# Optimization experiments

Measured on AMD Instinct MI355X. Metric: run time of the kernel, lower is better.

Reference implementation:

```python
import jax, jax.numpy as jnp
import numpy as np

N_NODES = 50000

def setup_inputs() -> dict:
    key = jax.random.key(0)
    k1, k2, k3, k4, k5 = jax.random.split(key, 5)
    x = jax.random.normal(k1, (50000, 512), dtype=jnp.float32)
    edge_row = jax.random.randint(k2, (800000,), 0, N_NODES, dtype=jnp.int64)
    edge_col = jax.random.randint(k3, (800000,), 0, N_NODES, dtype=jnp.int64)
    edge_val = jax.random.uniform(k4, (800000,), dtype=jnp.float32)
    # init like torch: uniform(-stdv, stdv), stdv = 1/sqrt(out_features)
    stdv = 1.0 / np.sqrt(96.0)
    weight = jax.random.uniform(k5, (512, 96), minval=-stdv, maxval=stdv, dtype=jnp.float32)
    return {"x": x, "edge_row": edge_row, "edge_col": edge_col, "edge_val": edge_val, "weight": weight}

def reference(x, edge_row, edge_col, edge_val, weight):
    # support = X @ W  -- dense GEMM [N, F_in] x [F_in, F_out]
    support = x @ weight
    # sparse adjacency matmul: out[row] += val * support[col]
    msgs = edge_val[:, None] * support[edge_col]          # [E, F_out]
    out = jax.ops.segment_sum(msgs, edge_row, num_segments=N_NODES)
    # act = ReLU (module default); bias=False
    return jax.nn.relu(out)
```

## Files before the change

kernel.cpp:

```cpp
#include <hip/hip_runtime.h>

#define N_NODES 50000
#define F_IN    512
#define F_OUT   96
#define N_EDGES 800000

#define RPB    128
#define NBKT   391
#define CAP    2560
#define ECHUNK 4096
#define NCHUNK ((N_EDGES + ECHUNK - 1) / ECHUNK)
#define GEMM_BLOCKS ((N_NODES + 63) / 64)

typedef __attribute__((ext_vector_type(8))) short bf16x8;
typedef __attribute__((ext_vector_type(4))) float f32x4;

__device__ __forceinline__ unsigned short f2bf(float f) {
    unsigned int u = __float_as_uint(f);
    unsigned int r = (u + 0x7FFFu + ((u >> 16) & 1u)) >> 16;
    return (unsigned short)r;
}
__device__ __forceinline__ float bf2f(unsigned short h) {
    return __uint_as_float(((unsigned int)h) << 16);
}

__global__ __launch_bounds__(256) void k_wcast(const float* __restrict__ w,
                                               unsigned short* __restrict__ wTq,
                                               int* __restrict__ bcnt) {
    if (blockIdx.x == 0) {
        const int t = threadIdx.x;
        bcnt[t] = 0;
        if (t < 144) bcnt[256 + t] = 0;
    }
    const int i = blockIdx.x * 256 + threadIdx.x;
    if (i < F_OUT * F_IN) {
        const int j    = i & 7;
        const int lane = (i >> 3) & 63;
        const int ks   = (i >> 9) & 1;
        const int tp   = i >> 10;
        const int t    = tp % 6;
        const int p    = tp / 6;
        const int lr   = lane & 15;
        const int kg   = lane >> 4;
        const int n    = t * 16 + lr;
        const int k    = p * 64 + ks * 32 + kg * 8 + j;
        wTq[i] = f2bf(w[(size_t)k * F_OUT + n]);
    }
}

__global__ __launch_bounds__(512) void k_fused(const float* __restrict__ x,
                                               const unsigned short* __restrict__ wTq,
                                               unsigned short* __restrict__ support,
                                               const int* __restrict__ erow,
                                               const int* __restrict__ ecol,
                                               const float* __restrict__ eval,
                                               int* __restrict__ bcnt,
                                               float2* __restrict__ bucket) {
    __shared__ __align__(16) char smem[16384];
    const int tid = threadIdx.x;

    if (blockIdx.x < NCHUNK) {
        int* hist  = (int*)smem;
        int* gbase = hist + 400;
        int* lcur  = gbase + 400;
        for (int i = tid; i < NBKT; i += 512) { hist[i] = 0; lcur[i] = 0; }
        __syncthreads();

        const int base = blockIdx.x * ECHUNK;
        const int n = min(ECHUNK, N_EDGES - base);

        for (int i = tid; i < n; i += 512)
            atomicAdd(&hist[erow[base + i] >> 7], 1);
        __syncthreads();

        for (int b = tid; b < NBKT; b += 512)
            gbase[b] = hist[b] ? atomicAdd(&bcnt[b], hist[b]) : 0;
        __syncthreads();

        for (int i = tid; i < n; i += 512) {
            const int r = erow[base + i];
            const int b = r >> 7;
            const int pos = gbase[b] + atomicAdd(&lcur[b], 1);
            if (pos >= 0 && pos < CAP)
                bucket[(size_t)b * CAP + pos] = make_float2(
                    __int_as_float(((r & 127) << 16) | ecol[base + i]),
                    eval[base + i]);
        }
        return;
    }

    unsigned short (*sX)[64 * 64] = (unsigned short (*)[64 * 64])smem;

    const int lane = tid & 63;
    const int wave = tid >> 6;
    const int wr   = wave & 3;
    const int wc   = wave >> 2;
    const int r0   = (blockIdx.x - NCHUNK) * 64;
    const int lr   = lane & 15;
    const int kg   = lane >> 4;

    f32x4 acc[3];
    #pragma unroll
    for (int t = 0; t < 3; ++t) acc[t] = (f32x4){0.f, 0.f, 0.f, 0.f};

    float4 xr[2];

    auto XLOAD = [&](int p) {
        #pragma unroll
        for (int i = 0; i < 2; ++i) {
            const int chunk = i * 512 + tid;
            const int row   = chunk >> 4;
            const int c     = chunk & 15;
            int gr = r0 + row;
            if (gr > N_NODES - 1) gr = N_NODES - 1;
            xr[i] = *reinterpret_cast<const float4*>(x + (size_t)gr * F_IN + p * 64 + c * 4);
        }
    };
    auto XWRITE = [&](int buf) {
        char* xb = (char*)&sX[buf][0];
        #pragma unroll
        for (int i = 0; i < 2; ++i) {
            const int chunk = i * 512 + tid;
            const int row   = chunk >> 4;
            const int c     = chunk & 15;
            ushort4 h;
            h.x = f2bf(xr[i].x); h.y = f2bf(xr[i].y);
            h.z = f2bf(xr[i].z); h.w = f2bf(xr[i].w);
            const int byte = (c * 8) ^ ((row & 7) << 4);
            *reinterpret_cast<ushort4*>(xb + row * 128 + byte) = h;
        }
    };
    auto COMPUTE = [&](int buf, int p) {
        const char* xb = (const char*)&sX[buf][0];
        const int xrow = wr * 16 + lr;
        const unsigned short* bbase = wTq + ((size_t)p * 12 + wc * 6) * 512 + lane * 8;
        #pragma unroll
        for (int ks = 0; ks < 2; ++ks) {
            const int off = (ks * 64 + kg * 16) ^ ((xrow & 7) << 4);
            const bf16x8 af = *reinterpret_cast<const bf16x8*>(xb + xrow * 128 + off);
            #pragma unroll
            for (int t = 0; t < 3; ++t) {
                const bf16x8 bq = *reinterpret_cast<const bf16x8*>(
                    bbase + (t * 2 + ks) * 512);
                acc[t] = __builtin_amdgcn_mfma_f32_16x16x32_bf16(af, bq, acc[t], 0, 0, 0);
            }
        }
    };

    XLOAD(0);
    XWRITE(0);
    __syncthreads();
    for (int p = 0; p < 8; ++p) {
        if (p < 7) XLOAD(p + 1);
        COMPUTE(p & 1, p);
        if (p < 7) XWRITE((p + 1) & 1);
        __syncthreads();
    }

    #pragma unroll
    for (int t = 0; t < 3; ++t) {
        #pragma unroll
        for (int r = 0; r < 4; ++r) {
            const int row = r0 + wr * 16 + kg * 4 + r;
            if (row < N_NODES)
                support[(size_t)row * F_OUT + wc * 48 + t * 16 + lr] = f2bf(acc[t][r]);
        }
    }
}

__global__ __launch_bounds__(256) void kS_sort(const int* __restrict__ bcnt,
                                               const float2* __restrict__ bucket,
                                               float2* __restrict__ bucket2,
                                               int* __restrict__ rowOffs) {
    __shared__ int cnt[RPB];
    __shared__ int sc[RPB];
    __shared__ int rbase[RPB];
    __shared__ int rcur[RPB];
    const int b   = blockIdx.x;
    const int tid = threadIdx.x;

    if (tid < RPB) { cnt[tid] = 0; rcur[tid] = 0; }
    __syncthreads();

    const int beg = b * CAP;
    const int n   = min(bcnt[b], CAP);

    for (int i = tid; i < n; i += 256)
        atomicAdd(&cnt[(__float_as_int(bucket[beg + i].x) >> 16) & 127], 1);
    __syncthreads();

    if (tid < RPB) sc[tid] = cnt[tid];
    __syncthreads();
    #pragma unroll
    for (int off = 1; off < RPB; off <<= 1) {
        int a = 0;
        if (tid < RPB && tid >= off) a = sc[tid - off];
        __syncthreads();
        if (tid < RPB) sc[tid] += a;
        __syncthreads();
    }
    if (tid < RPB) {
        const int rb = beg + sc[tid] - cnt[tid];
        rbase[tid] = rb;
        rowOffs[b * 129 + tid] = rb;
    }
    if (tid == RPB) rowOffs[b * 129 + RPB] = beg + n;
    __syncthreads();

    for (int i = tid; i < n; i += 256) {
        const float2 ev  = bucket[beg + i];
        const int    key = __float_as_int(ev.x);
        const int    r   = (key >> 16) & 127;
        const int    pos = rbase[r] + atomicAdd(&rcur[r], 1);
        bucket2[pos] = make_float2(__int_as_float(key & 0xFFFF), ev.y);
    }
}

__global__ __launch_bounds__(256) void k_gather(const int* __restrict__ rowOffs,
                                                const float2* __restrict__ bucket2,
                                                const unsigned short* __restrict__ support,
                                                float* __restrict__ out) {
    const int gid = blockIdx.x * 256 + threadIdx.x;
    if (gid >= N_NODES * 6) return;
    const int r   = gid / 6;
    const int f16 = gid - r * 6;

    const int idx = (r >> 7) * 129 + (r & 127);
    const int beg = rowOffs[idx];
    const int end = rowOffs[idx + 1];

    float acc[16];
    #pragma unroll
    for (int j = 0; j < 16; ++j) acc[j] = 0.f;

    for (int i = beg; i < end; ++i) {
        const float2 cv = bucket2[i];
        const int   c = __float_as_int(cv.x);
        const float v = cv.y;
        const unsigned short* sp = support + (size_t)c * F_OUT + f16 * 16;
        const bf16x8 s0 = *reinterpret_cast<const bf16x8*>(sp);
        const bf16x8 s1 = *reinterpret_cast<const bf16x8*>(sp + 8);
        #pragma unroll
        for (int j = 0; j < 8; ++j) {
            acc[j]     = fmaf(v, bf2f((unsigned short)s0[j]), acc[j]);
            acc[8 + j] = fmaf(v, bf2f((unsigned short)s1[j]), acc[8 + j]);
        }
    }

    float* o = out + (size_t)r * F_OUT + f16 * 16;
    #pragma unroll
    for (int q = 0; q < 4; ++q) {
        float4 ov;
        ov.x = fmaxf(acc[q * 4 + 0], 0.f);
        ov.y = fmaxf(acc[q * 4 + 1], 0.f);
        ov.z = fmaxf(acc[q * 4 + 2], 0.f);
        ov.w = fmaxf(acc[q * 4 + 3], 0.f);
        *reinterpret_cast<float4*>(o + q * 4) = ov;
    }
}

extern "C" void kernel_launch(void* const* d_in, const int* in_sizes, int n_in,
                              void* d_out, int out_size, void* d_ws, size_t ws_size,
                              hipStream_t stream) {
    const float* x    = (const float*)d_in[0];
    const int*   erow = (const int*)d_in[1];
    const int*   ecol = (const int*)d_in[2];
    const float* eval = (const float*)d_in[3];
    const float* w    = (const float*)d_in[4];
    float*       out  = (float*)d_out;

    unsigned short* support = (unsigned short*)d_ws;
    int*    bcnt    = (int*)((char*)d_ws + 9600000);
    int*    rowOffs = bcnt + 400;
    unsigned short* wTq = (unsigned short*)(rowOffs + 50560);
    float2* bucket  = (float2*)((char*)wTq + 98304);
    float2* bucket2 = bucket + (size_t)NBKT * CAP;

    k_wcast<<<(F_OUT * F_IN + 255) / 256, 256, 0, stream>>>(w, wTq, bcnt);

    k_fused<<<NCHUNK + GEMM_BLOCKS, 512, 0, stream>>>(x, wTq, support,
                                                      erow, ecol, eval,
                                                      bcnt, bucket);

    kS_sort<<<NBKT, 256, 0, stream>>>(bcnt, bucket, bucket2, rowOffs);

    const int gthreads = N_NODES * 6;
    k_gather<<<(gthreads + 255) / 256, 256, 0, stream>>>(rowOffs, bucket2, support, out);
}
```

Measured before the change: 82.09 us.

## Load GEMM A-fragments directly from global memory, dropping LDS staging

The dense X@W stage now has each wave own 16 full rows and all 96 output columns (6 accumulators), with 128 rows per block. A fragments are read straight from global memory in float and converted to bf16 in registers, with no shared-memory double buffering and no block barriers. This cuts LDS traffic, syncs and the smem footprint, which may raise occupancy. In exchange the global loads are strided per lane and less coalesced, there is no explicit prefetch pipelining, and each wave reloads all B fragments.

```diff
diff --git a/kernel.cpp b/kernel.cpp
--- a/kernel.cpp
+++ b/kernel.cpp
@@ -10,7 +10,7 @@
 #define CAP    2560
 #define ECHUNK 4096
 #define NCHUNK ((N_EDGES + ECHUNK - 1) / ECHUNK)
-#define GEMM_BLOCKS ((N_NODES + 63) / 64)
+#define GEMM_BLOCKS ((N_NODES + 127) / 128)
 
 typedef __attribute__((ext_vector_type(8))) short bf16x8;
 typedef __attribute__((ext_vector_type(4))) float f32x4;
@@ -56,13 +56,13 @@
                                                const float* __restrict__ eval,
                                                int* __restrict__ bcnt,
                                                float2* __restrict__ bucket) {
-    __shared__ __align__(16) char smem[16384];
+    __shared__ int smem[1200];
     const int tid = threadIdx.x;
 
     if (blockIdx.x < NCHUNK) {
-        int* hist  = (int*)smem;
-        int* gbase = hist + 400;
-        int* lcur  = gbase + 400;
+        int* hist  = smem;
+        int* gbase = smem + 400;
+        int* lcur  = smem + 800;
         for (int i = tid; i < NBKT; i += 512) { hist[i] = 0; lcur[i] = 0; }
         __syncthreads();
 
@@ -89,81 +89,49 @@
         return;
     }
 
-    unsigned short (*sX)[64 * 64] = (unsigned short (*)[64 * 64])smem;
-
     const int lane = tid & 63;
     const int wave = tid >> 6;
-    const int wr   = wave & 3;
-    const int wc   = wave >> 2;
-    const int r0   = (blockIdx.x - NCHUNK) * 64;
     const int lr   = lane & 15;
     const int kg   = lane >> 4;
 
-    f32x4 acc[3];
-    #pragma unroll
-    for (int t = 0; t < 3; ++t) acc[t] = (f32x4){0.f, 0.f, 0.f, 0.f};
-
-    float4 xr[2];
-
-    auto XLOAD = [&](int p) {
-        #pragma unroll
-        for (int i = 0; i < 2; ++i) {
-            const int chunk = i * 512 + tid;
-            const int row   = chunk >> 4;
-            const int c     = chunk & 15;
-            int gr = r0 + row;
-            if (gr > N_NODES - 1) gr = N_NODES - 1;
-            xr[i] = *reinterpret_cast<const float4*>(x + (size_t)gr * F_IN + p * 64 + c * 4);
-        }
-    };
-    auto XWRITE = [&](int buf) {
-        char* xb = (char*)&sX[buf][0];
-        #pragma unroll
-        for (int i = 0; i < 2; ++i) {
-            const int chunk = i * 512 + tid;
-            const int row   = chunk >> 4;
-            const int c     = chunk & 15;
-            ushort4 h;
-            h.x = f2bf(xr[i].x); h.y = f2bf(xr[i].y);
-            h.z = f2bf(xr[i].z); h.w = f2bf(xr[i].w);
-            const int byte = (c * 8) ^ ((row & 7) << 4);
-            *reinterpret_cast<ushort4*>(xb + row * 128 + byte) = h;
-        }
-    };
-    auto COMPUTE = [&](int buf, int p) {
-        const char* xb = (const char*)&sX[buf][0];
-        const int xrow = wr * 16 + lr;
-        const unsigned short* bbase = wTq + ((size_t)p * 12 + wc * 6) * 512 + lane * 8;
+    const int wrow0 = (blockIdx.x - NCHUNK) * 128 + wave * 16;
+    int grow = wrow0 + lr;
+    if (grow > N_NODES - 1) grow = N_NODES - 1;
+    const float* aptr = x + (size_t)grow * F_IN + kg * 8;
+    const unsigned short* bb = wTq + lane * 8;
+
+    f32x4 acc[6];
+    #pragma unroll
+    for (int t = 0; t < 6; ++t) acc[t] = (f32x4){0.f, 0.f, 0.f, 0.f};
+
+    #pragma unroll
+    for (int p = 0; p < 8; ++p) {
         #pragma unroll
         for (int ks = 0; ks < 2; ++ks) {
-            const int off = (ks * 64 + kg * 16) ^ ((xrow & 7) << 4);
-            const bf16x8 af = *reinterpret_cast<const bf16x8*>(xb + xrow * 128 + off);
+            const float* a = aptr + p * 64 + ks * 32;
+            const float4 a0 = *reinterpret_cast<const float4*>(a);
+            const float4 a1 = *reinterpret_cast<const float4*>(a + 4);
+            bf16x8 af;
+            af[0] = (short)f2bf(a0.x); af[1] = (short)f2bf(a0.y);
+            af[2] = (short)f2bf(a0.z); af[3] = (short)f2bf(a0.w);
+            af[4] = (short)f2bf(a1.x); af[5] = (short)f2bf(a1.y);
+            af[6] = (short)f2bf(a1.z); af[7] = (short)f2bf(a1.w);
             #pragma unroll
-            for (int t = 0; t < 3; ++t) {
-                const bf16x8 bq = *reinterpret_cast<const bf16x8*>(
-                    bbase + (t * 2 + ks) * 512);
+            for (int t = 0; t < 6; ++t) {
+                const int frag = p * 12 + t * 2 + ks;
+                const bf16x8 bq = *reinterpret_cast<const bf16x8*>(bb + (size_t)frag * 512);
                 acc[t] = __builtin_amdgcn_mfma_f32_16x16x32_bf16(af, bq, acc[t], 0, 0, 0);
             }
         }
-    };
-
-    XLOAD(0);
-    XWRITE(0);
-    __syncthreads();
-    for (int p = 0; p < 8; ++p) {
-        if (p < 7) XLOAD(p + 1);
-        COMPUTE(p & 1, p);
-        if (p < 7) XWRITE((p + 1) & 1);
-        __syncthreads();
-    }
-
-    #pragma unroll
-    for (int t = 0; t < 3; ++t) {
+    }
+
+    #pragma unroll
+    for (int t = 0; t < 6; ++t) {
         #pragma unroll
         for (int r = 0; r < 4; ++r) {
-            const int row = r0 + wr * 16 + kg * 4 + r;
+            const int row = wrow0 + kg * 4 + r;
             if (row < N_NODES)
-                support[(size_t)row * F_OUT + wc * 48 + t * 16 + lr] = f2bf(acc[t][r]);
+                support[(size_t)row * F_OUT + t * 16 + lr] = f2bf(acc[t][r]);
         }
     }
 }
```

Result: slower. 87.97 us (+7.2%).

## Split fused fill/GEMM kernel; fuse weight cast into bucket-fill kernel

Applied to the files above, without the earlier changes.

Moves the weight cast out of its own kernel and into the edge bucket-fill kernel as extra blocks, and splits the GEMM into a separate kernel with no branch. Counter zeroing becomes a tiny standalone kernel. This stops the GEMM blocks from sharing a launch with the fill blocks and gives the GEMM kernel a smaller, simpler body, at the cost of one more launch and no overlap between the fill and the GEMM.

```diff
diff --git a/kernel.cpp b/kernel.cpp
--- a/kernel.cpp
+++ b/kernel.cpp
@@ -10,6 +10,7 @@
 #define CAP    2560
 #define ECHUNK 4096
 #define NCHUNK ((N_EDGES + ECHUNK - 1) / ECHUNK)
+#define WCB    96
 #define GEMM_BLOCKS ((N_NODES + 63) / 64)
 
 typedef __attribute__((ext_vector_type(8))) short bf16x8;
@@ -24,70 +25,71 @@
     return __uint_as_float(((unsigned int)h) << 16);
 }
 
-__global__ __launch_bounds__(256) void k_wcast(const float* __restrict__ w,
-                                               unsigned short* __restrict__ wTq,
-                                               int* __restrict__ bcnt) {
-    if (blockIdx.x == 0) {
-        const int t = threadIdx.x;
-        bcnt[t] = 0;
-        if (t < 144) bcnt[256 + t] = 0;
-    }
-    const int i = blockIdx.x * 256 + threadIdx.x;
-    if (i < F_OUT * F_IN) {
-        const int j    = i & 7;
-        const int lane = (i >> 3) & 63;
-        const int ks   = (i >> 9) & 1;
-        const int tp   = i >> 10;
-        const int t    = tp % 6;
-        const int p    = tp / 6;
-        const int lr   = lane & 15;
-        const int kg   = lane >> 4;
-        const int n    = t * 16 + lr;
-        const int k    = p * 64 + ks * 32 + kg * 8 + j;
-        wTq[i] = f2bf(w[(size_t)k * F_OUT + n]);
-    }
-}
-
-__global__ __launch_bounds__(512) void k_fused(const float* __restrict__ x,
-                                               const unsigned short* __restrict__ wTq,
-                                               unsigned short* __restrict__ support,
-                                               const int* __restrict__ erow,
-                                               const int* __restrict__ ecol,
-                                               const float* __restrict__ eval,
-                                               int* __restrict__ bcnt,
-                                               float2* __restrict__ bucket) {
+__global__ __launch_bounds__(512) void k_zero(int* __restrict__ bcnt) {
+    if (threadIdx.x < 400) bcnt[threadIdx.x] = 0;
+}
+
+__global__ __launch_bounds__(512) void k_fillwcast(const int* __restrict__ erow,
+                                                   const int* __restrict__ ecol,
+                                                   const float* __restrict__ eval,
+                                                   int* __restrict__ bcnt,
+                                                   float2* __restrict__ bucket,
+                                                   const float* __restrict__ w,
+                                                   unsigned short* __restrict__ wTq) {
+    __shared__ int smem[1200];
+    const int tid = threadIdx.x;
+
+    if (blockIdx.x >= NCHUNK) {
+        const int i = (blockIdx.x - NCHUNK) * 512 + tid;
+        if (i < F_OUT * F_IN) {
+            const int j    = i & 7;
+            const int lane = (i >> 3) & 63;
+            const int ks   = (i >> 9) & 1;
+            const int tp   = i >> 10;
+            const int t    = tp % 6;
+            const int p    = tp / 6;
+            const int lr   = lane & 15;
+            const int kg   = lane >> 4;
+            const int n    = t * 16 + lr;
+            const int k    = p * 64 + ks * 32 + kg * 8 + j;
+            wTq[i] = f2bf(w[(size_t)k * F_OUT + n]);
+        }
+        return;
+    }
+
+    int* hist  = smem;
+    int* gbase = smem + 400;
+    int* lcur  = smem + 800;
+    for (int i = tid; i < NBKT; i += 512) { hist[i] = 0; lcur[i] = 0; }
+    __syncthreads();
+
+    const int base = blockIdx.x * ECHUNK;
+    const int n = min(ECHUNK, N_EDGES - base);
+
+    for (int i = tid; i < n; i += 512)
+        atomicAdd(&hist[erow[base + i] >> 7], 1);
+    __syncthreads();
+
+    for (int b = tid; b < NBKT; b += 512)
+        gbase[b] = hist[b] ? atomicAdd(&bcnt[b], hist[b]) : 0;
+    __syncthreads();
+
+    for (int i = tid; i < n; i += 512) {
+        const int r = erow[base + i];
+        const int b = r >> 7;
+        const int pos = gbase[b] + atomicAdd(&lcur[b], 1);
+        if (pos >= 0 && pos < CAP)
+            bucket[(size_t)b * CAP + pos] = make_float2(
+                __int_as_float(((r & 127) << 16) | ecol[base + i]),
+                eval[base + i]);
+    }
+}
+
+__global__ __launch_bounds__(512) void k_gemm(const float* __restrict__ x,
+                                              const unsigned short* __restrict__ wTq,
+                                              unsigned short* __restrict__ support) {
     __shared__ __align__(16) char smem[16384];
     const int tid = threadIdx.x;
-
-    if (blockIdx.x < NCHUNK) {
-        int* hist  = (int*)smem;
-        int* gbase = hist + 400;
-        int* lcur  = gbase + 400;
-        for (int i = tid; i < NBKT; i += 512) { hist[i] = 0; lcur[i] = 0; }
-        __syncthreads();
-
-        const int base = blockIdx.x * ECHUNK;
-        const int n = min(ECHUNK, N_EDGES - base);
-
-        for (int i = tid; i < n; i += 512)
-            atomicAdd(&hist[erow[base + i] >> 7], 1);
-        __syncthreads();
-
-        for (int b = tid; b < NBKT; b += 512)
-            gbase[b] = hist[b] ? atomicAdd(&bcnt[b], hist[b]) : 0;
-        __syncthreads();
-
-        for (int i = tid; i < n; i += 512) {
-            const int r = erow[base + i];
-            const int b = r >> 7;
-            const int pos = gbase[b] + atomicAdd(&lcur[b], 1);
-            if (pos >= 0 && pos < CAP)
-                bucket[(size_t)b * CAP + pos] = make_float2(
-                    __int_as_float(((r & 127) << 16) | ecol[base + i]),
-                    eval[base + i]);
-        }
-        return;
-    }
 
     unsigned short (*sX)[64 * 64] = (unsigned short (*)[64 * 64])smem;
 
@@ -95,7 +97,7 @@
     const int wave = tid >> 6;
     const int wr   = wave & 3;
     const int wc   = wave >> 2;
-    const int r0   = (blockIdx.x - NCHUNK) * 64;
+    const int r0   = blockIdx.x * 64;
     const int lr   = lane & 15;
     const int kg   = lane >> 4;
 
@@ -276,11 +278,12 @@
     float2* bucket  = (float2*)((char*)wTq + 98304);
     float2* bucket2 = bucket + (size_t)NBKT * CAP;
 
-    k_wcast<<<(F_OUT * F_IN + 255) / 256, 256, 0, stream>>>(w, wTq, bcnt);
-
-    k_fused<<<NCHUNK + GEMM_BLOCKS, 512, 0, stream>>>(x, wTq, support,
-                                                      erow, ecol, eval,
-                                                      bcnt, bucket);
+    k_zero<<<1, 512, 0, stream>>>(bcnt);
+
+    k_fillwcast<<<NCHUNK + WCB, 512, 0, stream>>>(erow, ecol, eval,
+                                                  bcnt, bucket, w, wTq);
+
+    k_gemm<<<GEMM_BLOCKS, 512, 0, stream>>>(x, wTq, support);
 
     kS_sort<<<NBKT, 256, 0, stream>>>(bcnt, bucket, bucket2, rowOffs);
 
```

After: 88.25 us. 7.5% more time.
